# Performance work log

Hardware: AMD Instinct MI355X
Metric: run time of the kernel (lower is better)

## Reference

```python
import jax, jax.numpy as jnp
import numpy as np

N = 50000      # nodes
E = 1600000    # edges (avg degree 32)
F_IN = 128     # num_features
DIM = 64       # hidden dim
L = 3          # num_gc_layers
G = 500        # graphs in batch


def setup_inputs() -> dict:
    key = jax.random.key(0)
    ks = jax.random.split(key, 16)
    inp = {}
    inp["x"] = jax.random.normal(ks[0], (N, F_IN), dtype=jnp.float32)
    inp["edge_index"] = jax.random.randint(ks[1], (2, E), 0, N, dtype=jnp.int32)
    inp["batch"] = jnp.sort(jax.random.randint(ks[2], (N,), 0, G, dtype=jnp.int32))
    # GIN layer MLP params: layer0 maps F_IN->DIM->DIM, later layers DIM->DIM->DIM
    d_in = F_IN
    ki = 3
    for i in range(L):
        inp[f"W1_{i}"] = jax.random.normal(ks[ki], (d_in, DIM), dtype=jnp.float32) / np.sqrt(d_in); ki += 1
        inp[f"b1_{i}"] = jnp.zeros((DIM,), dtype=jnp.float32)
        inp[f"W2_{i}"] = jax.random.normal(ks[ki], (DIM, DIM), dtype=jnp.float32) / np.sqrt(DIM); ki += 1
        inp[f"b2_{i}"] = jnp.zeros((DIM,), dtype=jnp.float32)
        d_in = DIM
    # final scoring head: concat readout -> dim * L inputs, 1 output
    inp["Wm"] = jax.random.normal(ks[ki], (DIM * L, 1), dtype=jnp.float32) / np.sqrt(DIM * L)
    inp["bm"] = jnp.zeros((1,), dtype=jnp.float32)
    return inp


def _segment_softmax(scores, seg, num_segments):
    # numerically stable softmax over elements grouped by seg; scores [M, 1]
    m = jax.ops.segment_max(scores, seg, num_segments=num_segments)
    e = jnp.exp(scores - m[seg])
    denom = jax.ops.segment_sum(e, seg, num_segments=num_segments)
    return e / denom[seg]


def _forward(x, edge_index, batch, params):
    src, dst = edge_index[0], edge_index[1]
    n = x.shape[0]
    xs = []
    h = x
    for i in range(L):
        W1, b1, W2, b2 = params[4 * i: 4 * i + 4]
        # GINConv (eps=0): h_i <- MLP(h_i + sum_{j->i} h_j)
        agg = jax.ops.segment_sum(h[src], dst, num_segments=n)
        h = jax.nn.relu((h + agg) @ W1 + b1) @ W2 + b2
        if i != L - 1:
            h = jax.nn.relu(h)
        xs.append(h)
    node_prob = jnp.concatenate(xs, axis=1)            # concat readout [N, DIM*L]
    Wm, bm = params[4 * L], params[4 * L + 1]
    node_score = node_prob @ Wm + bm                   # [N, 1]
    # lift_node_score_to_edge_score
    src_score = node_score[src]                        # [E, 1]
    dst_score = node_score[dst]
    edge_score = src_score * dst_score
    edge_prop = _segment_softmax(edge_score, dst, n)   # softmax over edges per dst
    new_score = jax.ops.segment_sum(src_score * edge_prop, dst, num_segments=n)
    node_score = node_score + new_score
    # final softmax over nodes grouped by graph id
    return _segment_softmax(node_score, batch, G)


def reference(x, edge_index, batch, W1_0, b1_0, W2_0, b2_0, W1_1, b1_1, W2_1, b2_1,
              W1_2, b1_2, W2_2, b2_2, Wm, bm):
    params = [W1_0, b1_0, W2_0, b2_0, W1_1, b1_1, W2_1, b2_1,
              W1_2, b1_2, W2_2, b2_2, Wm, bm]
    return _forward(x, edge_index, batch, params)
```

## Files before the change

### kernel.cpp

```cpp
#include <hip/hip_runtime.h>
#include <hip/hip_fp16.h>
#include <math.h>

#define N_NODES 50000
#define N_EDGES 1600000
#define N_GRAPH 500
#define CHUNKS 128
#define EPC (N_EDGES / CHUNKS)
#define NP1 (N_NODES + 1)
#define NIT ((EPC + 1023) / 1024)

__device__ __forceinline__ float rl(float v, int k) {
    return __int_as_float(__builtin_amdgcn_readlane(__float_as_int(v), k));
}
__device__ __forceinline__ void hacc16(float4& A, float4& B, uint4 w) {
    float2 f0 = __half22float2(*reinterpret_cast<__half2*>(&w.x));
    float2 f1 = __half22float2(*reinterpret_cast<__half2*>(&w.y));
    float2 f2 = __half22float2(*reinterpret_cast<__half2*>(&w.z));
    float2 f3 = __half22float2(*reinterpret_cast<__half2*>(&w.w));
    A.x += f0.x; A.y += f0.y; A.z += f1.x; A.w += f1.y;
    B.x += f2.x; B.y += f2.y; B.z += f3.x; B.w += f3.y;
}

__global__ __launch_bounds__(1024) void histsort_kernel(const int* __restrict__ src,
                                                        const int* __restrict__ dst,
                                                        int* __restrict__ csrc_chunk,
                                                        unsigned short* __restrict__ locs) {
    __shared__ unsigned packed[N_NODES / 2];
    __shared__ unsigned aux[1024];
    const int c = blockIdx.x;
    const int s0 = c * EPC;
    const int tid = threadIdx.x;

    for (int i = tid; i < N_NODES / 2; i += 1024) packed[i] = 0;
    __syncthreads();

    unsigned short lrv[NIT];
#pragma unroll
    for (int it = 0; it < NIT; it++) {
        int e = s0 + it * 1024 + tid;
        if (e < s0 + EPC) {
            int d = dst[e];
            int sh = (d & 1) * 16;
            unsigned old = atomicAdd(&packed[d >> 1], 1u << sh);
            lrv[it] = (unsigned short)((old >> sh) & 0xffffu);
        }
    }
    __syncthreads();

    const int W = 25;
    int w0 = tid * W;
    int w1 = min(w0 + W, N_NODES / 2);
    unsigned run = 0;
    for (int i = w0; i < w1; i++) {
        unsigned v = packed[i];
        unsigned lo = v & 0xffffu, hi = v >> 16;
        packed[i] = run | ((run + lo) << 16);
        run += lo + hi;
    }
    aux[tid] = run;
    __syncthreads();
    for (int off = 1; off < 1024; off <<= 1) {
        unsigned t = (tid >= off) ? aux[tid - off] : 0;
        __syncthreads();
        aux[tid] += t;
        __syncthreads();
    }
    unsigned b0 = (tid == 0) ? 0 : aux[tid - 1];
    if (b0) {
        unsigned addv = b0 | (b0 << 16);
        for (int i = w0; i < w1; i++) packed[i] += addv;
    }
    __syncthreads();

    int* outc = csrc_chunk + (size_t)c * EPC;
#pragma unroll
    for (int it = 0; it < NIT; it++) {
        int e = s0 + it * 1024 + tid;
        if (e < s0 + EPC) {
            int d = dst[e];
            unsigned pw = packed[d >> 1];
            unsigned loc = (d & 1) ? (pw >> 16) : (pw & 0xffffu);
            outc[loc + lrv[it]] = src[e];
        }
    }
    unsigned short* lc = locs + (size_t)c * NP1;
    for (int d = tid; d <= N_NODES; d += 1024) {
        unsigned short loc;
        if (d == N_NODES) {
            loc = (unsigned short)EPC;
        } else {
            unsigned pw = packed[d >> 1];
            loc = (unsigned short)((d & 1) ? (pw >> 16) : (pw & 0xffffu));
        }
        lc[d] = loc;
    }
}

__global__ __launch_bounds__(1024) void base_scan1_kernel(const unsigned short* __restrict__ locs,
                                                          unsigned short* __restrict__ base,
                                                          int* __restrict__ deg,
                                                          int* __restrict__ part, int N) {
    int d = blockIdx.x * 1024 + threadIdx.x;
    int run = 0;
    if (d < N) {
#pragma unroll 8
        for (int c = 0; c < CHUNKS; c++) {
            int l0 = locs[(size_t)c * NP1 + d];
            int l1 = locs[(size_t)c * NP1 + d + 1];
            base[(size_t)c * N + d] = (unsigned short)run;
            run += l1 - l0;
        }
        deg[d] = run;
    }
    int v = run;
#pragma unroll
    for (int o = 32; o >= 1; o >>= 1) v += __shfl_xor(v, o);
    __shared__ int red[16];
    if ((threadIdx.x & 63) == 0) red[threadIdx.x >> 6] = v;
    __syncthreads();
    if (threadIdx.x == 0) {
        int s = 0;
#pragma unroll
        for (int k = 0; k < 16; k++) s += red[k];
        part[blockIdx.x] = s;
    }
}

__global__ __launch_bounds__(1024) void scan3_kernel(const int* __restrict__ deg,
                                                     const int* __restrict__ part,
                                                     int* __restrict__ rowptr, int N, int nb) {
    __shared__ int blockOff;
    __shared__ int wsum[16];
    int lane = threadIdx.x & 63;
    int w = threadIdx.x >> 6;
    if (threadIdx.x < 64) {
        int pv = (lane < nb && lane < (int)blockIdx.x) ? part[lane] : 0;
#pragma unroll
        for (int o = 32; o >= 1; o >>= 1) pv += __shfl_xor(pv, o);
        if (lane == 0) blockOff = pv;
    }
    int i = blockIdx.x * 1024 + threadIdx.x;
    int v = (i < N) ? deg[i] : 0;
    int inc = v;
#pragma unroll
    for (int o = 1; o < 64; o <<= 1) {
        int t = __shfl_up(inc, o);
        if (lane >= o) inc += t;
    }
    if (lane == 63) wsum[w] = inc;
    __syncthreads();
    if (threadIdx.x < 16) {
        int x = wsum[threadIdx.x];
        int xo = x;
#pragma unroll
        for (int o = 1; o < 16; o <<= 1) {
            int t = __shfl_up(x, o);
            if ((int)threadIdx.x >= o) x += t;
        }
        wsum[threadIdx.x] = x - xo;
    }
    __syncthreads();
    int b = blockOff + wsum[w];
    if (i < N) {
        rowptr[i] = b + inc - v;
        if (i == N - 1) rowptr[N] = b + inc;
    }
}

__global__ __launch_bounds__(256) void gatherfill_kernel(const int* __restrict__ csrc_chunk,
                                                         const unsigned short* __restrict__ locs,
                                                         const unsigned short* __restrict__ base,
                                                         const int* __restrict__ rowptr,
                                                         int* __restrict__ csr_src) {
    const int perXcd = N_NODES / 8;
    int xcd = blockIdx.x & 7;
    int idx = (blockIdx.x >> 3) * 4 + (threadIdx.x >> 6);
    if (idx >= perXcd) return;
    int wid = xcd * perXcd + idx;
    int lane = threadIdx.x & 63;
    int rp = rowptr[wid];
#pragma unroll
    for (int cc = 0; cc < 2; cc++) {
        int c = lane + cc * 64;
        const unsigned short* lc = locs + (size_t)c * NP1;
        int l0 = lc[wid];
        int l1 = lc[wid + 1];
        int cnt = l1 - l0;
        int ob = rp + (int)base[(size_t)c * N_NODES + wid];
        const int* in = csrc_chunk + (size_t)c * EPC + l0;
        for (int i = 0; i < cnt; i++) csr_src[ob + i] = in[i];
    }
}

__global__ __launch_bounds__(256) void gemm0_kernel(const float* __restrict__ x,
                                                    const float* __restrict__ W1,
                                                    __half* __restrict__ y0,
                                                    int N, int totalWaves) {
    int lane = threadIdx.x & 63;
    int wid = (blockIdx.x * 256 + threadIdx.x) >> 6;
    float wA[64], wB[64];
#pragma unroll
    for (int k = 0; k < 64; k++) wA[k] = W1[k * 64 + lane];
#pragma unroll
    for (int k = 0; k < 64; k++) wB[k] = W1[(64 + k) * 64 + lane];
    for (int node = wid; node < N; node += totalWaves) {
        float xa = x[(size_t)node * 128 + lane];
        float xb = x[(size_t)node * 128 + 64 + lane];
        float a0 = 0.f, a1 = 0.f, a2 = 0.f, a3 = 0.f;
#pragma unroll
        for (int k = 0; k < 64; k += 4) {
            a0 = fmaf(rl(xa, k + 0), wA[k + 0], a0);
            a1 = fmaf(rl(xa, k + 1), wA[k + 1], a1);
            a2 = fmaf(rl(xa, k + 2), wA[k + 2], a2);
            a3 = fmaf(rl(xa, k + 3), wA[k + 3], a3);
        }
#pragma unroll
        for (int k = 0; k < 64; k += 4) {
            a0 = fmaf(rl(xb, k + 0), wB[k + 0], a0);
            a1 = fmaf(rl(xb, k + 1), wB[k + 1], a1);
            a2 = fmaf(rl(xb, k + 2), wB[k + 2], a2);
            a3 = fmaf(rl(xb, k + 3), wB[k + 3], a3);
        }
        y0[(size_t)node * 64 + lane] = __float2half((a0 + a1) + (a2 + a3));
    }
}

__global__ __launch_bounds__(256) void agg_kernel(const __half* __restrict__ yh,
                                                  const int* __restrict__ rowptr,
                                                  const int* __restrict__ csr_src,
                                                  float* __restrict__ u, int N) {
    int wid = (blockIdx.x * 256 + threadIdx.x) >> 6;
    int lane = threadIdx.x & 63;
    if (wid >= N) return;
    int q = lane >> 3;
    int r = lane & 7;
    int start = rowptr[wid];
    int end = rowptr[wid + 1];
    float4 A = make_float4(0.f, 0.f, 0.f, 0.f);
    float4 B = make_float4(0.f, 0.f, 0.f, 0.f);
    int j = start;
    for (; j + 64 <= end; j += 64) {
        int s0 = csr_src[j + q];
        int s1 = csr_src[j + 8 + q];
        int s2 = csr_src[j + 16 + q];
        int s3 = csr_src[j + 24 + q];
        int s4 = csr_src[j + 32 + q];
        int s5 = csr_src[j + 40 + q];
        int s6 = csr_src[j + 48 + q];
        int s7 = csr_src[j + 56 + q];
        uint4 w0 = *(const uint4*)(yh + (size_t)s0 * 64 + r * 8);
        uint4 w1 = *(const uint4*)(yh + (size_t)s1 * 64 + r * 8);
        uint4 w2 = *(const uint4*)(yh + (size_t)s2 * 64 + r * 8);
        uint4 w3 = *(const uint4*)(yh + (size_t)s3 * 64 + r * 8);
        uint4 w4 = *(const uint4*)(yh + (size_t)s4 * 64 + r * 8);
        uint4 w5 = *(const uint4*)(yh + (size_t)s5 * 64 + r * 8);
        uint4 w6 = *(const uint4*)(yh + (size_t)s6 * 64 + r * 8);
        uint4 w7 = *(const uint4*)(yh + (size_t)s7 * 64 + r * 8);
        hacc16(A, B, w0); hacc16(A, B, w1); hacc16(A, B, w2); hacc16(A, B, w3);
        hacc16(A, B, w4); hacc16(A, B, w5); hacc16(A, B, w6); hacc16(A, B, w7);
    }
#pragma unroll
    for (int m = 0; m < 8; m++) {
        int e = j + 8 * m + q;
        if (e < end) {
            int s = csr_src[e];
            uint4 w = *(const uint4*)(yh + (size_t)s * 64 + r * 8);
            hacc16(A, B, w);
        }
    }
#pragma unroll
    for (int o = 8; o <= 32; o <<= 1) {
        A.x += __shfl_xor(A.x, o); A.y += __shfl_xor(A.y, o);
        A.z += __shfl_xor(A.z, o); A.w += __shfl_xor(A.w, o);
        B.x += __shfl_xor(B.x, o); B.y += __shfl_xor(B.y, o);
        B.z += __shfl_xor(B.z, o); B.w += __shfl_xor(B.w, o);
    }
    if (lane < 8) {
        uint4 w = *(const uint4*)(yh + (size_t)wid * 64 + r * 8);
        hacc16(A, B, w);
        *(float4*)(u + (size_t)wid * 64 + r * 8) = A;
        *(float4*)(u + (size_t)wid * 64 + r * 8 + 4) = B;
    }
}

template <int LAYER>
__global__ __launch_bounds__(256) void mlpAB_kernel(const float* __restrict__ u,
                                                    const float* __restrict__ b1,
                                                    const float* __restrict__ W2,
                                                    const float* __restrict__ b2,
                                                    const float* __restrict__ W1n,
                                                    const float* __restrict__ Wm,
                                                    __half* __restrict__ ynext,
                                                    float* __restrict__ score,
                                                    int N, int totalWaves) {
    int lane = threadIdx.x & 63;
    int wid = (blockIdx.x * 256 + threadIdx.x) >> 6;
    float w2[64], w1[64];
#pragma unroll
    for (int k = 0; k < 64; k++) w2[k] = W2[k * 64 + lane];
#pragma unroll
    for (int k = 0; k < 64; k++) w1[k] = W1n[k * 64 + lane];
    float bb1 = b1[lane], bb2 = b2[lane], wm = Wm[LAYER * 64 + lane];

    int node = wid;
    float uin = (node < N) ? u[(size_t)node * 64 + lane] : 0.f;
    for (; node < N; node += totalWaves) {
        int nn = node + totalWaves;
        float unext = (nn < N) ? u[(size_t)nn * 64 + lane] : 0.f;
        float t = fmaxf(uin + bb1, 0.f);
        float a0 = 0.f, a1 = 0.f, a2 = 0.f, a3 = 0.f;
#pragma unroll
        for (int k = 0; k < 64; k += 4) {
            a0 = fmaf(rl(t, k + 0), w2[k + 0], a0);
            a1 = fmaf(rl(t, k + 1), w2[k + 1], a1);
            a2 = fmaf(rl(t, k + 2), w2[k + 2], a2);
            a3 = fmaf(rl(t, k + 3), w2[k + 3], a3);
        }
        float h = fmaxf(bb2 + ((a0 + a1) + (a2 + a3)), 0.f);
        float p = h * wm;
#pragma unroll
        for (int o = 32; o >= 1; o >>= 1) p += __shfl_xor(p, o);
        if (lane == 0) {
            if (LAYER == 0) score[node] = p;
            else score[node] += p;
        }
        float y0 = 0.f, y1 = 0.f, y2 = 0.f, y3 = 0.f;
#pragma unroll
        for (int k = 0; k < 64; k += 4) {
            y0 = fmaf(rl(h, k + 0), w1[k + 0], y0);
            y1 = fmaf(rl(h, k + 1), w1[k + 1], y1);
            y2 = fmaf(rl(h, k + 2), w1[k + 2], y2);
            y3 = fmaf(rl(h, k + 3), w1[k + 3], y3);
        }
        ynext[(size_t)node * 64 + lane] = __float2half((y0 + y1) + (y2 + y3));
        uin = unext;
    }
}

__global__ __launch_bounds__(256) void mlpA2_kernel(const float* __restrict__ u,
                                                    const float* __restrict__ b1,
                                                    const float* __restrict__ W2,
                                                    const float* __restrict__ b2,
                                                    const float* __restrict__ Wm,
                                                    float* __restrict__ score,
                                                    int N, int totalWaves) {
    int lane = threadIdx.x & 63;
    int wid = (blockIdx.x * 256 + threadIdx.x) >> 6;
    float w2[64];
#pragma unroll
    for (int k = 0; k < 64; k++) w2[k] = W2[k * 64 + lane];
    float bb1 = b1[lane], bb2 = b2[lane], wm = Wm[2 * 64 + lane];

    int node = wid;
    float uin = (node < N) ? u[(size_t)node * 64 + lane] : 0.f;
    for (; node < N; node += totalWaves) {
        int nn = node + totalWaves;
        float unext = (nn < N) ? u[(size_t)nn * 64 + lane] : 0.f;
        float t = fmaxf(uin + bb1, 0.f);
        float a0 = 0.f, a1 = 0.f, a2 = 0.f, a3 = 0.f;
#pragma unroll
        for (int k = 0; k < 64; k += 4) {
            a0 = fmaf(rl(t, k + 0), w2[k + 0], a0);
            a1 = fmaf(rl(t, k + 1), w2[k + 1], a1);
            a2 = fmaf(rl(t, k + 2), w2[k + 2], a2);
            a3 = fmaf(rl(t, k + 3), w2[k + 3], a3);
        }
        float h = bb2 + ((a0 + a1) + (a2 + a3));
        float p = h * wm;
#pragma unroll
        for (int o = 32; o >= 1; o >>= 1) p += __shfl_xor(p, o);
        if (lane == 0) score[node] += p;
        uin = unext;
    }
}

__global__ __launch_bounds__(256) void edge_softmax_kernel(const float* __restrict__ score,
                                                           const int* __restrict__ rowptr,
                                                           const int* __restrict__ csr_src,
                                                           const float* __restrict__ bm,
                                                           float* __restrict__ nsf, int N) {
    int wid = (blockIdx.x * blockDim.x + threadIdx.x) >> 6;
    int lane = threadIdx.x & 63;
    if (wid >= N) return;
    float b = bm[0];
    float sd = score[wid] + b;
    int start = rowptr[wid];
    int end = rowptr[wid + 1];
    bool has0 = (start + lane < end);
    float ss0 = 0.f;
    float m = -INFINITY;
    if (has0) {
        ss0 = score[csr_src[start + lane]] + b;
        m = ss0 * sd;
    }
    for (int j = start + 64 + lane; j < end; j += 64) {
        float ss = score[csr_src[j]] + b;
        m = fmaxf(m, ss * sd);
    }
#pragma unroll
    for (int o = 32; o >= 1; o >>= 1) m = fmaxf(m, __shfl_xor(m, o));
    float se = 0.f, swe = 0.f;
    if (m > -INFINITY) {
        if (has0) {
            float e0 = expf(ss0 * sd - m);
            se += e0;
            swe += ss0 * e0;
        }
        for (int j = start + 64 + lane; j < end; j += 64) {
            float ss = score[csr_src[j]] + b;
            float e = expf(ss * sd - m);
            se += e;
            swe += ss * e;
        }
#pragma unroll
        for (int o = 32; o >= 1; o >>= 1) {
            se += __shfl_xor(se, o);
            swe += __shfl_xor(swe, o);
        }
    }
    float ns = (se > 0.f) ? (swe / se) : 0.f;
    if (lane == 0) nsf[wid] = sd + ns;
}

__global__ __launch_bounds__(256) void graph_softmax_kernel(const float* __restrict__ nsf,
                                                            const int* __restrict__ batch,
                                                            float* __restrict__ out, int N) {
    int g = blockIdx.x;
    int tid = threadIdx.x;
    int lo = 0, hi = N;
    while (lo < hi) { int mid = (lo + hi) >> 1; if (batch[mid] < g) lo = mid + 1; else hi = mid; }
    int s0 = lo;
    hi = N;
    while (lo < hi) { int mid = (lo + hi) >> 1; if (batch[mid] < g + 1) lo = mid + 1; else hi = mid; }
    int s1 = lo;

    __shared__ float red[4];
    __shared__ float bval;
    float m = -INFINITY;
    for (int i = s0 + tid; i < s1; i += 256) m = fmaxf(m, nsf[i]);
#pragma unroll
    for (int o = 32; o >= 1; o >>= 1) m = fmaxf(m, __shfl_xor(m, o));
    if ((tid & 63) == 0) red[tid >> 6] = m;
    __syncthreads();
    if (tid == 0) bval = fmaxf(fmaxf(red[0], red[1]), fmaxf(red[2], red[3]));
    __syncthreads();
    float bmx = bval;
    float s = 0.f;
    for (int i = s0 + tid; i < s1; i += 256) {
        float e = expf(nsf[i] - bmx);
        out[i] = e;
        s += e;
    }
#pragma unroll
    for (int o = 32; o >= 1; o >>= 1) s += __shfl_xor(s, o);
    __syncthreads();
    if ((tid & 63) == 0) red[tid >> 6] = s;
    __syncthreads();
    if (tid == 0) bval = red[0] + red[1] + red[2] + red[3];
    __syncthreads();
    float inv = 1.f / bval;
    for (int i = s0 + tid; i < s1; i += 256) out[i] *= inv;
}

extern "C" void kernel_launch(void* const* d_in, const int* in_sizes, int n_in,
                              void* d_out, int out_size, void* d_ws, size_t ws_size,
                              hipStream_t stream) {
    const int N = N_NODES, E = N_EDGES;

    const float* x = (const float*)d_in[0];
    const int* ei = (const int*)d_in[1];
    const int* batch = (const int*)d_in[2];
    const float* W1a[3] = {(const float*)d_in[3], (const float*)d_in[7], (const float*)d_in[11]};
    const float* b1a[3] = {(const float*)d_in[4], (const float*)d_in[8], (const float*)d_in[12]};
    const float* W2a[3] = {(const float*)d_in[5], (const float*)d_in[9], (const float*)d_in[13]};
    const float* b2a[3] = {(const float*)d_in[6], (const float*)d_in[10], (const float*)d_in[14]};
    const float* Wm = (const float*)d_in[15];
    const float* bm = (const float*)d_in[16];
    float* out = (float*)d_out;

    const int* srcp = ei;
    const int* dstp = ei + E;

    float* ubuf = (float*)d_ws;
    int* csrc_chunk = (int*)ubuf;
    __half* yA = (__half*)(ubuf + (size_t)N * 64);
    __half* yB = yA + (size_t)N * 64;
    float* score = (float*)(yB + (size_t)N * 64);
    float* nsf = score + N;
    int* deg = (int*)(nsf + N);
    int* rowptr = deg + N;
    int* part = rowptr + N + 1;
    int* csr_src = part + 64;
    unsigned short* locs = (unsigned short*)(csr_src + E);
    unsigned short* base = locs + (size_t)CHUNKS * NP1;

    histsort_kernel<<<CHUNKS, 1024, 0, stream>>>(srcp, dstp, csrc_chunk, locs);

    const int nbScan = (N + 1023) / 1024;
    base_scan1_kernel<<<nbScan, 1024, 0, stream>>>(locs, base, deg, part, N);
    scan3_kernel<<<nbScan, 1024, 0, stream>>>(deg, part, rowptr, N, nbScan);

    const int gfBlocks = 8 * ((N / 8 + 3) / 4);
    gatherfill_kernel<<<gfBlocks, 256, 0, stream>>>(csrc_chunk, locs, base, rowptr, csr_src);

    const int gw = 4096;
    gemm0_kernel<<<1024, 256, 0, stream>>>(x, W1a[0], yA, N, gw);

    int aggBlocks = (N + 3) / 4;

    agg_kernel<<<aggBlocks, 256, 0, stream>>>(yA, rowptr, csr_src, ubuf, N);
    mlpAB_kernel<0><<<1024, 256, 0, stream>>>(ubuf, b1a[0], W2a[0], b2a[0], W1a[1], Wm, yB, score, N, gw);

    agg_kernel<<<aggBlocks, 256, 0, stream>>>(yB, rowptr, csr_src, ubuf, N);
    mlpAB_kernel<1><<<1024, 256, 0, stream>>>(ubuf, b1a[1], W2a[1], b2a[1], W1a[2], Wm, yA, score, N, gw);

    agg_kernel<<<aggBlocks, 256, 0, stream>>>(yA, rowptr, csr_src, ubuf, N);
    mlpA2_kernel<<<1024, 256, 0, stream>>>(ubuf, b1a[2], W2a[2], b2a[2], Wm, score, N, gw);

    edge_softmax_kernel<<<(N + 3) / 4, 256, 0, stream>>>(score, rowptr, csr_src, bm, nsf, N);

    graph_softmax_kernel<<<N_GRAPH, 256, 0, stream>>>(nsf, batch, out, N);
}
```

Baseline: 349.0 us.

## Split histogram sort per chunk into two node-range halves across blocks

The CSR-building histogram sort now launches two blocks per edge chunk, each handling only destinations in one half of the node range. Each block needs half as much shared memory for the packed counters, which allows more blocks in flight and doubles the block count so more compute units are busy. The downstream scan and gather kernels are reindexed to the new per-half offset layout. In exchange, each chunk's dst array is read twice and the scratch buffer for sorted sources doubles in size.

```diff
diff --git a/kernel.cpp b/kernel.cpp
--- a/kernel.cpp
+++ b/kernel.cpp
@@ -9,6 +9,8 @@
 #define EPC (N_EDGES / CHUNKS)
 #define NP1 (N_NODES + 1)
 #define NIT ((EPC + 1023) / 1024)
+#define HALF_N (N_NODES / 2)
+#define HNP1 (HALF_N + 1)
 
 __device__ __forceinline__ float rl(float v, int k) {
     return __int_as_float(__builtin_amdgcn_readlane(__float_as_int(v), k));
@@ -26,13 +28,15 @@
                                                         const int* __restrict__ dst,
                                                         int* __restrict__ csrc_chunk,
                                                         unsigned short* __restrict__ locs) {
-    __shared__ unsigned packed[N_NODES / 2];
+    __shared__ unsigned packed[HALF_N / 2];
     __shared__ unsigned aux[1024];
-    const int c = blockIdx.x;
+    const int c = blockIdx.x >> 1;
+    const int h = blockIdx.x & 1;
+    const int lo = h * HALF_N;
     const int s0 = c * EPC;
     const int tid = threadIdx.x;
 
-    for (int i = tid; i < N_NODES / 2; i += 1024) packed[i] = 0;
+    for (int i = tid; i < HALF_N / 2; i += 1024) packed[i] = 0;
     __syncthreads();
 
     unsigned short lrv[NIT];
@@ -41,22 +45,25 @@
         int e = s0 + it * 1024 + tid;
         if (e < s0 + EPC) {
             int d = dst[e];
-            int sh = (d & 1) * 16;
-            unsigned old = atomicAdd(&packed[d >> 1], 1u << sh);
-            lrv[it] = (unsigned short)((old >> sh) & 0xffffu);
-        }
-    }
-    __syncthreads();
-
-    const int W = 25;
+            int ld = d - lo;
+            if (ld >= 0 && ld < HALF_N) {
+                int sh = (ld & 1) * 16;
+                unsigned old = atomicAdd(&packed[ld >> 1], 1u << sh);
+                lrv[it] = (unsigned short)((old >> sh) & 0xffffu);
+            }
+        }
+    }
+    __syncthreads();
+
+    const int W = 13;
     int w0 = tid * W;
-    int w1 = min(w0 + W, N_NODES / 2);
+    int w1 = min(w0 + W, HALF_N / 2);
     unsigned run = 0;
     for (int i = w0; i < w1; i++) {
         unsigned v = packed[i];
-        unsigned lo = v & 0xffffu, hi = v >> 16;
-        packed[i] = run | ((run + lo) << 16);
-        run += lo + hi;
+        unsigned plo = v & 0xffffu, phi = v >> 16;
+        packed[i] = run | ((run + plo) << 16);
+        run += plo + phi;
     }
     aux[tid] = run;
     __syncthreads();
@@ -72,28 +79,32 @@
         for (int i = w0; i < w1; i++) packed[i] += addv;
     }
     __syncthreads();
-
-    int* outc = csrc_chunk + (size_t)c * EPC;
+    unsigned total = aux[1023];
+
+    int* outc = csrc_chunk + (size_t)(c * 2 + h) * EPC;
 #pragma unroll
     for (int it = 0; it < NIT; it++) {
         int e = s0 + it * 1024 + tid;
         if (e < s0 + EPC) {
             int d = dst[e];
-            unsigned pw = packed[d >> 1];
-            unsigned loc = (d & 1) ? (pw >> 16) : (pw & 0xffffu);
-            outc[loc + lrv[it]] = src[e];
-        }
-    }
-    unsigned short* lc = locs + (size_t)c * NP1;
-    for (int d = tid; d <= N_NODES; d += 1024) {
-        unsigned short loc;
-        if (d == N_NODES) {
-            loc = (unsigned short)EPC;
+            int ld = d - lo;
+            if (ld >= 0 && ld < HALF_N) {
+                unsigned pw = packed[ld >> 1];
+                unsigned loc = (ld & 1) ? (pw >> 16) : (pw & 0xffffu);
+                outc[loc + lrv[it]] = src[e];
+            }
+        }
+    }
+    unsigned short* lc = locs + (size_t)(c * 2 + h) * HNP1;
+    for (int ld = tid; ld <= HALF_N; ld += 1024) {
+        unsigned short v;
+        if (ld == HALF_N) {
+            v = (unsigned short)total;
         } else {
-            unsigned pw = packed[d >> 1];
-            loc = (unsigned short)((d & 1) ? (pw >> 16) : (pw & 0xffffu));
-        }
-        lc[d] = loc;
+            unsigned pw = packed[ld >> 1];
+            v = (unsigned short)((ld & 1) ? (pw >> 16) : (pw & 0xffffu));
+        }
+        lc[ld] = v;
     }
 }
 
@@ -104,10 +115,13 @@
     int d = blockIdx.x * 1024 + threadIdx.x;
     int run = 0;
     if (d < N) {
+        int h = (d >= HALF_N) ? 1 : 0;
+        int ld = d - h * HALF_N;
 #pragma unroll 8
         for (int c = 0; c < CHUNKS; c++) {
-            int l0 = locs[(size_t)c * NP1 + d];
-            int l1 = locs[(size_t)c * NP1 + d + 1];
+            const unsigned short* lc = locs + (size_t)(c * 2 + h) * HNP1;
+            int l0 = lc[ld];
+            int l1 = lc[ld + 1];
             base[(size_t)c * N + d] = (unsigned short)run;
             run += l1 - l0;
         }
@@ -179,16 +193,18 @@
     if (idx >= perXcd) return;
     int wid = xcd * perXcd + idx;
     int lane = threadIdx.x & 63;
+    int h = (wid >= HALF_N) ? 1 : 0;
+    int ld = wid - h * HALF_N;
     int rp = rowptr[wid];
 #pragma unroll
     for (int cc = 0; cc < 2; cc++) {
         int c = lane + cc * 64;
-        const unsigned short* lc = locs + (size_t)c * NP1;
-        int l0 = lc[wid];
-        int l1 = lc[wid + 1];
+        const unsigned short* lc = locs + (size_t)(c * 2 + h) * HNP1;
+        int l0 = lc[ld];
+        int l1 = lc[ld + 1];
         int cnt = l1 - l0;
         int ob = rp + (int)base[(size_t)c * N_NODES + wid];
-        const int* in = csrc_chunk + (size_t)c * EPC + l0;
+        const int* in = csrc_chunk + (size_t)(c * 2 + h) * EPC + l0;
         for (int i = 0; i < cnt; i++) csr_src[ob + i] = in[i];
     }
 }
@@ -493,9 +509,9 @@
     int* part = rowptr + N + 1;
     int* csr_src = part + 64;
     unsigned short* locs = (unsigned short*)(csr_src + E);
-    unsigned short* base = locs + (size_t)CHUNKS * NP1;
-
-    histsort_kernel<<<CHUNKS, 1024, 0, stream>>>(srcp, dstp, csrc_chunk, locs);
+    unsigned short* base = locs + (size_t)2 * CHUNKS * HNP1;
+
+    histsort_kernel<<<CHUNKS * 2, 1024, 0, stream>>>(srcp, dstp, csrc_chunk, locs);
 
     const int nbScan = (N + 1023) / 1024;
     base_scan1_kernel<<<nbScan, 1024, 0, stream>>>(locs, base, deg, part, N);
```

Result: faster. 342.0 us (-2.0%).
